# Kernel optimization log

Measured on AMD Instinct MI355X. Metric: run time of the kernel, lower is better.

The kernel has to match this reference:

```python
import jax, jax.numpy as jnp
import numpy as np

NUM_EMBEDDINGS = 2048
EMBEDDING_DIM = 256
COMMITMENT_COST = 0.25


def setup_inputs() -> dict:
    key = jax.random.key(0)
    k1, k2 = jax.random.split(key)
    z_e = jax.random.normal(k1, (64, EMBEDDING_DIM, 32, 32), dtype=jnp.float32)
    # nn.Embedding weight initialized uniform(-1/K, 1/K)
    bound = 1.0 / NUM_EMBEDDINGS
    codebook = jax.random.uniform(k2, (NUM_EMBEDDINGS, EMBEDDING_DIM),
                                  dtype=jnp.float32, minval=-bound, maxval=bound)
    return {"z_e": z_e, "codebook": codebook}


def reference(z_e, codebook):
    B, C, H, W = z_e.shape  # C == embedding_dim
    K = codebook.shape[0]
    sg = jax.lax.stop_gradient

    # [B, C, H, W] -> [B*H*W, C]
    z_e_flat = jnp.transpose(z_e, (0, 2, 3, 1)).reshape(-1, C)

    # squared L2 distances: ||z||^2 - 2 z E^T + ||E||^2  -> [N, K]
    distances = (jnp.sum(z_e_flat ** 2, axis=1, keepdims=True)
                 - 2.0 * jnp.matmul(z_e_flat, codebook.T)
                 + jnp.sum(codebook ** 2, axis=1))
    indices = jnp.argmin(distances, axis=1)  # [N]

    encodings = jax.nn.one_hot(indices, K, dtype=z_e_flat.dtype)  # [N, K]
    z_q_flat = codebook[indices]  # [N, C] embedding gather
    z_q = jnp.transpose(z_q_flat.reshape(B, H, W, C), (0, 3, 1, 2))

    codebook_loss = jnp.mean((z_q_flat - sg(z_e_flat)) ** 2)
    commitment_loss = jnp.mean((sg(z_q_flat) - z_e_flat) ** 2)
    loss = codebook_loss + COMMITMENT_COST * commitment_loss

    e_mean = jnp.mean(encodings, axis=0)  # [K]
    perplexity = jnp.exp(-jnp.sum(e_mean * jnp.log(e_mean + 1e-10)))

    # straight-through estimator
    z_q_st = z_e + sg(z_q - z_e)
    return z_q_st, loss, perplexity, encodings
```

## Files before the change

### kernel.cpp

```cpp
#include <hip/hip_runtime.h>
#include <hip/hip_bf16.h>
#include <math.h>

#define NTOT 65536
#define KCB  2048
#define CDIM 256
#define HW   1024

#define OUT_LOSS 16777216
#define OUT_PERP 16777217
#define OUT_ENC  16777218

#define ZB_OFF_F  16777232
#define CBB_OFF_F 33554448

#define WS_SROW 0
#define WS_CK   262144
#define WS_IDX  270336
#define WS_CNT  532480
#define WS_PART 540672

#define MARGIN 3e-3f
#define CAP 4096

typedef __attribute__((ext_vector_type(8))) short short8;
typedef __attribute__((ext_vector_type(4))) float f32x4;

__device__ inline unsigned enc_f(float x) {
    unsigned u = __float_as_uint(x);
    return (u & 0x80000000u) ? ~u : (u | 0x80000000u);
}
__device__ inline float dec_f(unsigned e) {
    unsigned u = (e & 0x80000000u) ? (e ^ 0x80000000u) : ~e;
    return __uint_as_float(u);
}

__device__ inline void lds_min_u64(unsigned long long* p, unsigned long long v) {
    unsigned long long old = *p;
    while (v < old) {
        unsigned long long assumed = old;
        old = atomicCAS(p, assumed, v);
        if (old == assumed) break;
    }
}

__global__ __launch_bounds__(256) void k_prep(const float* __restrict__ z, const float* __restrict__ cb,
                                              ushort* __restrict__ zb, ushort* __restrict__ cbb,
                                              float* __restrict__ ck, float* __restrict__ srow,
                                              int* __restrict__ cntK) {
    __shared__ float tile[64][65];
    const int tid = threadIdx.x;
    const int bid = blockIdx.x;
    if (bid < 512) {
        int wv = tid >> 6, lane = tid & 63;
        int r = bid * 4 + wv;
        const float* row = cb + (size_t)r * CDIM;
        float4 v = *(const float4*)(row + lane * 4);
        ushort4 o;
        __hip_bfloat16 h;
        h = __float2bfloat16(v.x); o.x = *(ushort*)&h;
        h = __float2bfloat16(v.y); o.y = *(ushort*)&h;
        h = __float2bfloat16(v.z); o.z = *(ushort*)&h;
        h = __float2bfloat16(v.w); o.w = *(ushort*)&h;
        *(ushort4*)(cbb + (size_t)r * CDIM + lane * 4) = o;
        float s = v.x*v.x + v.y*v.y + v.z*v.z + v.w*v.w;
        for (int off = 32; off >= 1; off >>= 1) s += __shfl_down(s, off, 64);
        if (lane == 0) ck[r] = s;
        if (lane == 1) cntK[r] = 0;
    } else if (bid < 768) {
        int n = (bid - 512) * 256 + tid;
        int b = n >> 10, hw = n & 1023;
        const float* base = z + (size_t)b * (CDIM * HW) + hw;
        float s = 0.f;
#pragma unroll 8
        for (int c = 0; c < CDIM; ++c) { float v = base[(size_t)c * HW]; s = fmaf(v, v, s); }
        srow[n] = s;
    } else {
        int zbid = bid - 768;
        int hwT = zbid & 15, cT = (zbid >> 4) & 3, b = zbid >> 6;
        int c0 = cT * 64, hw0 = hwT * 64;
        int w = tid >> 6, hw = tid & 63;
#pragma unroll
        for (int l = 0; l < 16; ++l) {
            int c = l * 4 + w;
            tile[c][hw] = z[((size_t)b * CDIM + (c0 + c)) * HW + hw0 + hw];
        }
        __syncthreads();
        int r = tid >> 2, g = tid & 3;
        union { ushort u[16]; int4 v[2]; } pk;
#pragma unroll
        for (int j = 0; j < 16; ++j) {
            __hip_bfloat16 h = __float2bfloat16(tile[g * 16 + j][r]);
            pk.u[j] = *(ushort*)&h;
        }
        size_t n = (size_t)b * HW + hw0 + r;
        ushort* dst = zb + n * CDIM + c0 + g * 16;
        *(int4*)(dst) = pk.v[0];
        *(int4*)(dst + 8) = pk.v[1];
    }
}

__device__ __forceinline__ void tile_mfma(const ushort* __restrict__ cbb, int kb, int col, int quad,
                                          const short8 (&areg)[4][8], f32x4 (&acc)[4][2]) {
#pragma unroll
    for (int nt = 0; nt < 4; ++nt)
#pragma unroll
        for (int kt = 0; kt < 2; ++kt)
            acc[nt][kt] = (f32x4){0.f, 0.f, 0.f, 0.f};
#pragma unroll
    for (int kt = 0; kt < 2; ++kt) {
        short8 bfrag[8];
#pragma unroll
        for (int cs = 0; cs < 8; ++cs)
            bfrag[cs] = *(const short8*)(cbb + ((size_t)(kb + kt * 16 + col)) * CDIM + cs * 32 + quad * 8);
#pragma unroll
        for (int nt = 0; nt < 4; ++nt)
#pragma unroll
            for (int cs = 0; cs < 8; ++cs)
                acc[nt][kt] = __builtin_amdgcn_mfma_f32_16x16x32_bf16(areg[nt][cs], bfrag[cs], acc[nt][kt], 0, 0, 0);
    }
}

__global__ __launch_bounds__(256, 2) void k_mfma_argmin(
    const ushort* __restrict__ zb, const ushort* __restrict__ cbb,
    const float* __restrict__ z, const float* __restrict__ cb,
    const float* __restrict__ srow, const float* __restrict__ ckg,
    int* __restrict__ indices, int* __restrict__ cntK)
{
    __shared__ unsigned rowminU[64];
    __shared__ int   candRK[CAP];
    __shared__ float candD[CAP];
    __shared__ int   cnt;
    __shared__ float thrF[64];
    __shared__ unsigned long long best[64];

    const int tid = threadIdx.x;
    const int w = tid >> 6, lane = tid & 63;
    const int col = lane & 15, quad = lane >> 4;
    const int n0 = blockIdx.x * 64;

    short8 areg[4][8];
#pragma unroll
    for (int nt = 0; nt < 4; ++nt)
#pragma unroll
        for (int cs = 0; cs < 8; ++cs)
            areg[nt][cs] = *(const short8*)(zb + ((size_t)(n0 + nt * 16 + col)) * CDIM + cs * 32 + quad * 8);

    if (tid < 64) { rowminU[tid] = 0xFFFFFFFFu; best[tid] = ~0ull; }
    if (tid == 0) cnt = 0;
    float gmin[16];
#pragma unroll
    for (int s = 0; s < 16; ++s) gmin[s] = INFINITY;
    __syncthreads();

    {
        f32x4 acc[4][2];
        tile_mfma(cbb, w * 32, col, quad, areg, acc);
#pragma unroll
        for (int kt = 0; kt < 2; ++kt) {
            const float ckv = ckg[w * 32 + kt * 16 + col];
#pragma unroll
            for (int nt = 0; nt < 4; ++nt)
#pragma unroll
                for (int r = 0; r < 4; ++r) {
                    float dt = fmaf(-2.0f, acc[nt][kt][r], ckv);
                    const int s = nt * 4 + r;
                    if (dt < gmin[s]) {
                        gmin[s] = dt;
                        atomicMin(&rowminU[nt * 16 + quad * 4 + r], enc_f(dt));
                    }
                }
        }
    }
    __syncthreads();

    int npass = 1;
    float thr[16];
    for (int pass = 0; pass < npass; ++pass) {
        for (int k0 = 0; k0 < KCB; k0 += 128) {
            const int kb = k0 + w * 32;
            if (pass == 0) {
#pragma unroll
                for (int s = 0; s < 16; ++s) {
                    int row = (s >> 2) * 16 + quad * 4 + (s & 3);
                    gmin[s] = fminf(gmin[s], dec_f(rowminU[row]));
                }
            }
            f32x4 acc[4][2];
            tile_mfma(cbb, kb, col, quad, areg, acc);
#pragma unroll
            for (int kt = 0; kt < 2; ++kt) {
                const int k = kb + kt * 16 + col;
                const float ckv = ckg[k];
#pragma unroll
                for (int nt = 0; nt < 4; ++nt)
#pragma unroll
                    for (int r = 0; r < 4; ++r) {
                        float dt = fmaf(-2.0f, acc[nt][kt][r], ckv);
                        const int s = nt * 4 + r;
                        const int row = nt * 16 + quad * 4 + r;
                        if (pass == 0) {
                            if (dt < gmin[s]) {
                                gmin[s] = dt;
                                atomicMin(&rowminU[row], enc_f(dt));
                            }
                            if (dt <= gmin[s] + MARGIN) {
                                int p = atomicAdd(&cnt, 1);
                                if (p < CAP) { candRK[p] = (row << 16) | k; candD[p] = dt; }
                            }
                        } else if (dt <= thr[s]) {
                            int p = atomicAdd(&cnt, 1);
                            if (p < CAP) { candRK[p] = (row << 16) | k; candD[p] = dt; }
                        }
                    }
            }
        }
        __syncthreads();
        if (pass == 0) {
#pragma unroll
            for (int s = 0; s < 16; ++s)
                thr[s] = dec_f(rowminU[(s >> 2) * 16 + quad * 4 + (s & 3)]) + MARGIN;
            if (cnt > CAP) {
                npass = 2;
                __syncthreads();
                if (tid == 0) cnt = 0;
                __syncthreads();
            }
        }
    }
    if (tid < 64) thrF[tid] = dec_f(rowminU[tid]) + MARGIN;
    __syncthreads();

    const int b = n0 >> 10, hw0 = n0 & 1023;
    const int nc = min(cnt, CAP);
    for (int t = tid; t < nc; t += 256) {
        const int rc = candRK[t];
        const int row = rc >> 16, k = rc & 0xFFFF;
        if (candD[t] > thrF[row]) continue;
        const float* zp = z + (size_t)b * (CDIM * HW) + hw0 + row;
        const float* cp = cb + (size_t)k * CDIM;
        float m = 0.f;
#pragma unroll 8
        for (int c = 0; c < CDIM; ++c) m = fmaf(zp[(size_t)c << 10], cp[c], m);
        float d = (srow[n0 + row] - 2.0f * m) + ckg[k];
        unsigned long long pk = ((unsigned long long)__float_as_uint(d) << 32) | (unsigned)k;
        lds_min_u64(&best[row], pk);
    }
    __syncthreads();
    if (tid < 64) {
        int bk = (int)(best[tid] & 0xFFFFFFFFull);
        indices[n0 + tid] = bk;
        atomicAdd(&cntK[bk], 1);
    }
}

__global__ __launch_bounds__(256, 2) void k_gather(const float* __restrict__ z, const float* __restrict__ cb,
                                                   const int* __restrict__ idx, float* __restrict__ out0,
                                                   double* __restrict__ part) {
    __shared__ float qt[CDIM * 64];
    __shared__ double sh[256];
    const int tid = threadIdx.x;
    const int nl = tid & 63, cg = tid >> 6;
    const int n0 = blockIdx.x * 64;
    const int b = n0 >> 10, hw0 = n0 & 1023;
    const int k = idx[n0 + nl];
    const float* crow = cb + (size_t)k * CDIM + cg * 64;
#pragma unroll
    for (int j4 = 0; j4 < 16; ++j4) {
        float4 v = *(const float4*)(crow + j4 * 4);
        int c = cg * 64 + j4 * 4;
        qt[(c + 0) * 64 + nl] = v.x;
        qt[(c + 1) * 64 + nl] = v.y;
        qt[(c + 2) * 64 + nl] = v.z;
        qt[(c + 3) * 64 + nl] = v.w;
    }
    __syncthreads();
    double acc = 0.0;
    const size_t ebase = ((size_t)b * CDIM) * HW + hw0 + nl;
#pragma unroll 4
    for (int j = 0; j < 64; ++j) {
        int c = cg * 64 + j;
        size_t e = ebase + ((size_t)c << 10);
        float ze = z[e];
        float q = qt[c * 64 + nl];
        float d = q - ze;
        out0[e] = ze + d;
        acc += (double)d * (double)d;
    }
    sh[tid] = acc;
    __syncthreads();
    for (int s = 128; s > 0; s >>= 1) {
        if (tid < s) sh[tid] += sh[tid + s];
        __syncthreads();
    }
    if (tid == 0) part[blockIdx.x] = sh[0];
}

__global__ __launch_bounds__(256) void k_encodings(const int* __restrict__ idx, float4* __restrict__ p4,
                                                   float* __restrict__ tail) {
    __shared__ int sidx[17];
    const int tid = threadIdx.x;
    const size_t g0 = (size_t)blockIdx.x * 8192;
    const long f0 = 4L * (long)g0 - 2;
    int nlo = (int)(f0 >> 11); if (nlo < 0) nlo = 0;
    if (tid < 17) { int n = nlo + tid; sidx[tid] = (n < NTOT) ? idx[n] : -1; }
    __syncthreads();
    const float4 zv = make_float4(0.f, 0.f, 0.f, 0.f);
    for (int i = 0; i < 32; ++i) {
        size_t g = g0 + (size_t)i * 256 + tid;
        long fe = 4L * (long)g - 2;
        float4 v = zv;
        if (fe < 0) {
            int kk = sidx[0];
            if (kk == 0) v.z = 1.f;
            if (kk == 1) v.w = 1.f;
        } else {
            int n = (int)(fe >> 11);
            int k0c = (int)(fe & 2047);
            if (k0c >= 2045) {
#pragma unroll
                for (int j = 0; j < 4; ++j) {
                    long fej = fe + j;
                    int nj = (int)(fej >> 11);
                    int kj = (int)(fej & 2047);
                    int li = nj - nlo;
                    int kk = (li >= 0 && li < 17) ? sidx[li] : -2;
                    ((float*)&v)[j] = (kk == kj) ? 1.f : 0.f;
                }
            } else {
                int d = sidx[n - nlo] - k0c;
                if (d >= 0 && d < 4) ((float*)&v)[d] = 1.f;
            }
        }
        p4[g] = v;
    }
    if (blockIdx.x == 0 && tid == 0) {
        int kk = idx[NTOT - 1];
        tail[0] = (kk == 2046) ? 1.f : 0.f;
        tail[1] = (kk == 2047) ? 1.f : 0.f;
    }
}

__global__ __launch_bounds__(256) void k_finalize(const double* __restrict__ part, const int* __restrict__ cnt,
                                                  float* __restrict__ out) {
    __shared__ double sh[256];
    double a = 0.0;
    for (int i = threadIdx.x; i < 1024; i += 256) a += part[i];
    sh[threadIdx.x] = a; __syncthreads();
    for (int s = 128; s > 0; s >>= 1) { if (threadIdx.x < s) sh[threadIdx.x] += sh[threadIdx.x + s]; __syncthreads(); }
    double total = sh[0];
    __syncthreads();
    double p = 0.0;
    for (int i = threadIdx.x; i < 2048; i += 256) {
        double pm = (double)cnt[i] / 65536.0;
        p += pm * log(pm + 1e-10);
    }
    sh[threadIdx.x] = p; __syncthreads();
    for (int s = 128; s > 0; s >>= 1) { if (threadIdx.x < s) sh[threadIdx.x] += sh[threadIdx.x + s]; __syncthreads(); }
    if (threadIdx.x == 0) {
        double mean = total / ((double)NTOT * (double)CDIM);
        out[OUT_LOSS] = (float)(mean * 1.25);
        out[OUT_PERP] = (float)exp(-sh[0]);
    }
}

extern "C" void kernel_launch(void* const* d_in, const int* in_sizes, int n_in,
                              void* d_out, int out_size, void* d_ws, size_t ws_size,
                              hipStream_t stream) {
    const float* z  = (const float*)d_in[0];
    const float* cb = (const float*)d_in[1];
    float* out = (float*)d_out;
    char* ws = (char*)d_ws;
    float*  srow = (float*)(ws + WS_SROW);
    float*  ck   = (float*)(ws + WS_CK);
    int*    idx  = (int*)(ws + WS_IDX);
    int*    cnt  = (int*)(ws + WS_CNT);
    double* part = (double*)(ws + WS_PART);
    ushort* zb  = (ushort*)(out + ZB_OFF_F);
    ushort* cbb = (ushort*)(out + CBB_OFF_F);

    hipLaunchKernelGGL(k_prep,        dim3(4864), dim3(256), 0, stream, z, cb, zb, cbb, ck, srow, cnt);
    hipLaunchKernelGGL(k_mfma_argmin, dim3(1024), dim3(256), 0, stream, zb, cbb, z, cb, srow, ck, idx, cnt);
    hipLaunchKernelGGL(k_gather,      dim3(1024), dim3(256), 0, stream, z, cb, idx, out, part);
    hipLaunchKernelGGL(k_encodings,   dim3(4096), dim3(256), 0, stream, idx, (float4*)(out + OUT_LOSS),
                       out + (OUT_LOSS + (size_t)33554432 * 4));
    hipLaunchKernelGGL(k_finalize,    dim3(1),    dim3(256), 0, stream, part, cnt, out);
}
```

Before: 1.004 ms.

## Replace two-pass candidate scan with per-lane top-2 tracking and single MFMA pass

The approximate argmin kernel no longer uses a warm-up tile plus shared-memory atomicMin updates and per-element candidate appends inside the MFMA loop. Each lane now keeps the best and second-best distance and index per row in registers. Rows are reduced with shuffles and per-wave shared slots to build a threshold, and candidates are emitted only afterward: the best index alone, or all 32 of the lane's column indices when the second-best lies within the margin. This removes atomics and branches from the hot loop, halves the candidate buffer and drops candD. The cost is a heavier fallback: a full fp32 exact scan over all 2048 codes for the block when candidates overflow.

```diff
diff --git a/kernel.cpp b/kernel.cpp
--- a/kernel.cpp
+++ b/kernel.cpp
@@ -21,7 +21,7 @@
 #define WS_PART 540672
 
 #define MARGIN 3e-3f
-#define CAP 4096
+#define CAP 2048
 
 typedef __attribute__((ext_vector_type(8))) short short8;
 typedef __attribute__((ext_vector_type(4))) float f32x4;
@@ -100,38 +100,17 @@
     }
 }
 
-__device__ __forceinline__ void tile_mfma(const ushort* __restrict__ cbb, int kb, int col, int quad,
-                                          const short8 (&areg)[4][8], f32x4 (&acc)[4][2]) {
-#pragma unroll
-    for (int nt = 0; nt < 4; ++nt)
-#pragma unroll
-        for (int kt = 0; kt < 2; ++kt)
-            acc[nt][kt] = (f32x4){0.f, 0.f, 0.f, 0.f};
-#pragma unroll
-    for (int kt = 0; kt < 2; ++kt) {
-        short8 bfrag[8];
-#pragma unroll
-        for (int cs = 0; cs < 8; ++cs)
-            bfrag[cs] = *(const short8*)(cbb + ((size_t)(kb + kt * 16 + col)) * CDIM + cs * 32 + quad * 8);
-#pragma unroll
-        for (int nt = 0; nt < 4; ++nt)
-#pragma unroll
-            for (int cs = 0; cs < 8; ++cs)
-                acc[nt][kt] = __builtin_amdgcn_mfma_f32_16x16x32_bf16(areg[nt][cs], bfrag[cs], acc[nt][kt], 0, 0, 0);
-    }
-}
-
 __global__ __launch_bounds__(256, 2) void k_mfma_argmin(
     const ushort* __restrict__ zb, const ushort* __restrict__ cbb,
     const float* __restrict__ z, const float* __restrict__ cb,
     const float* __restrict__ srow, const float* __restrict__ ckg,
     int* __restrict__ indices, int* __restrict__ cntK)
 {
-    __shared__ unsigned rowminU[64];
+    __shared__ unsigned long long wmin[4][64];
+    __shared__ float thrRow[64];
     __shared__ int   candRK[CAP];
-    __shared__ float candD[CAP];
     __shared__ int   cnt;
-    __shared__ float thrF[64];
+    __shared__ int   allscan;
     __shared__ unsigned long long best[64];
 
     const int tid = threadIdx.x;
@@ -146,97 +125,95 @@
         for (int cs = 0; cs < 8; ++cs)
             areg[nt][cs] = *(const short8*)(zb + ((size_t)(n0 + nt * 16 + col)) * CDIM + cs * 32 + quad * 8);
 
-    if (tid < 64) { rowminU[tid] = 0xFFFFFFFFu; best[tid] = ~0ull; }
-    if (tid == 0) cnt = 0;
-    float gmin[16];
-#pragma unroll
-    for (int s = 0; s < 16; ++s) gmin[s] = INFINITY;
-    __syncthreads();
-
-    {
-        f32x4 acc[4][2];
-        tile_mfma(cbb, w * 32, col, quad, areg, acc);
+    float m1[16], m2[16]; int k1[16];
+#pragma unroll
+    for (int s = 0; s < 16; ++s) { m1[s] = INFINITY; m2[s] = INFINITY; k1[s] = 0; }
+
+    for (int k0 = 0; k0 < KCB; k0 += 128) {
+        const int kb = k0 + w * 32;
 #pragma unroll
         for (int kt = 0; kt < 2; ++kt) {
-            const float ckv = ckg[w * 32 + kt * 16 + col];
+            const int kk = kb + kt * 16 + col;
+            const ushort* bbase = cbb + (size_t)kk * CDIM + quad * 8;
+            short8 bfrag[8];
+#pragma unroll
+            for (int cs = 0; cs < 8; ++cs) bfrag[cs] = *(const short8*)(bbase + cs * 32);
+            f32x4 acc[4];
+#pragma unroll
+            for (int nt = 0; nt < 4; ++nt) acc[nt] = (f32x4){0.f, 0.f, 0.f, 0.f};
+#pragma unroll
+            for (int cs = 0; cs < 8; ++cs)
+#pragma unroll
+                for (int nt = 0; nt < 4; ++nt)
+                    acc[nt] = __builtin_amdgcn_mfma_f32_16x16x32_bf16(areg[nt][cs], bfrag[cs], acc[nt], 0, 0, 0);
+            const float ckv = ckg[kk];
 #pragma unroll
             for (int nt = 0; nt < 4; ++nt)
 #pragma unroll
                 for (int r = 0; r < 4; ++r) {
-                    float dt = fmaf(-2.0f, acc[nt][kt][r], ckv);
+                    float dt = fmaf(-2.0f, acc[nt][r], ckv);
                     const int s = nt * 4 + r;
-                    if (dt < gmin[s]) {
-                        gmin[s] = dt;
-                        atomicMin(&rowminU[nt * 16 + quad * 4 + r], enc_f(dt));
-                    }
+                    bool c = dt < m1[s];
+                    m2[s] = fminf(m2[s], fmaxf(dt, m1[s]));
+                    m1[s] = fminf(m1[s], dt);
+                    k1[s] = c ? kk : k1[s];
                 }
         }
     }
-    __syncthreads();
-
-    int npass = 1;
-    float thr[16];
-    for (int pass = 0; pass < npass; ++pass) {
-        for (int k0 = 0; k0 < KCB; k0 += 128) {
-            const int kb = k0 + w * 32;
-            if (pass == 0) {
-#pragma unroll
-                for (int s = 0; s < 16; ++s) {
-                    int row = (s >> 2) * 16 + quad * 4 + (s & 3);
-                    gmin[s] = fminf(gmin[s], dec_f(rowminU[row]));
+
+#pragma unroll
+    for (int s = 0; s < 16; ++s) {
+        unsigned long long v = ((unsigned long long)enc_f(m1[s]) << 32) | (unsigned)k1[s];
+#pragma unroll
+        for (int m = 1; m <= 8; m <<= 1) {
+            unsigned long long o = __shfl_xor(v, m, 64);
+            v = (o < v) ? o : v;
+        }
+        if (col == 0) wmin[w][(s >> 2) * 16 + quad * 4 + (s & 3)] = v;
+    }
+    if (tid == 0) { cnt = 0; allscan = 0; }
+    if (tid < 64) best[tid] = ~0ull;
+    __syncthreads();
+    if (tid < 64) {
+        unsigned long long v = wmin[0][tid];
+        unsigned long long o = wmin[1][tid]; v = (o < v) ? o : v;
+        o = wmin[2][tid]; v = (o < v) ? o : v;
+        o = wmin[3][tid]; v = (o < v) ? o : v;
+        thrRow[tid] = dec_f((unsigned)(v >> 32)) + MARGIN;
+    }
+    __syncthreads();
+
+#pragma unroll
+    for (int s = 0; s < 16; ++s) {
+        const int row = (s >> 2) * 16 + quad * 4 + (s & 3);
+        const float thr = thrRow[row];
+        if (m1[s] <= thr) {
+            int p = atomicAdd(&cnt, 1);
+            if (p < CAP) candRK[p] = (row << 16) | k1[s];
+        }
+        if (m2[s] <= thr) {
+            const int kt = s & 1;
+            (void)kt;
+            int p = atomicAdd(&cnt, 32);
+            if (p + 32 <= CAP) {
+#pragma unroll
+                for (int k0i = 0; k0i < 16; ++k0i) {
+                    int kbase = k0i * 128 + w * 32 + col;
+                    candRK[p + 2 * k0i]     = (row << 16) | kbase;
+                    candRK[p + 2 * k0i + 1] = (row << 16) | (kbase + 16);
                 }
             }
-            f32x4 acc[4][2];
-            tile_mfma(cbb, kb, col, quad, areg, acc);
-#pragma unroll
-            for (int kt = 0; kt < 2; ++kt) {
-                const int k = kb + kt * 16 + col;
-                const float ckv = ckg[k];
-#pragma unroll
-                for (int nt = 0; nt < 4; ++nt)
-#pragma unroll
-                    for (int r = 0; r < 4; ++r) {
-                        float dt = fmaf(-2.0f, acc[nt][kt][r], ckv);
-                        const int s = nt * 4 + r;
-                        const int row = nt * 16 + quad * 4 + r;
-                        if (pass == 0) {
-                            if (dt < gmin[s]) {
-                                gmin[s] = dt;
-                                atomicMin(&rowminU[row], enc_f(dt));
-                            }
-                            if (dt <= gmin[s] + MARGIN) {
-                                int p = atomicAdd(&cnt, 1);
-                                if (p < CAP) { candRK[p] = (row << 16) | k; candD[p] = dt; }
-                            }
-                        } else if (dt <= thr[s]) {
-                            int p = atomicAdd(&cnt, 1);
-                            if (p < CAP) { candRK[p] = (row << 16) | k; candD[p] = dt; }
-                        }
-                    }
-            }
-        }
-        __syncthreads();
-        if (pass == 0) {
-#pragma unroll
-            for (int s = 0; s < 16; ++s)
-                thr[s] = dec_f(rowminU[(s >> 2) * 16 + quad * 4 + (s & 3)]) + MARGIN;
-            if (cnt > CAP) {
-                npass = 2;
-                __syncthreads();
-                if (tid == 0) cnt = 0;
-                __syncthreads();
-            }
-        }
-    }
-    if (tid < 64) thrF[tid] = dec_f(rowminU[tid]) + MARGIN;
-    __syncthreads();
+        }
+    }
+    __syncthreads();
+    if (cnt > CAP) { if (tid == 0) allscan = 1; }
+    __syncthreads();
+    const int nc = allscan ? 0 : min(cnt, CAP);
 
     const int b = n0 >> 10, hw0 = n0 & 1023;
-    const int nc = min(cnt, CAP);
     for (int t = tid; t < nc; t += 256) {
         const int rc = candRK[t];
         const int row = rc >> 16, k = rc & 0xFFFF;
-        if (candD[t] > thrF[row]) continue;
         const float* zp = z + (size_t)b * (CDIM * HW) + hw0 + row;
         const float* cp = cb + (size_t)k * CDIM;
         float m = 0.f;
@@ -245,6 +222,22 @@
         float d = (srow[n0 + row] - 2.0f * m) + ckg[k];
         unsigned long long pk = ((unsigned long long)__float_as_uint(d) << 32) | (unsigned)k;
         lds_min_u64(&best[row], pk);
+    }
+    if (allscan) {
+        for (int row = 0; row < 64; ++row) {
+            const float sr = srow[n0 + row];
+            const float* zp = z + (size_t)b * (CDIM * HW) + hw0 + row;
+            for (int kq = 0; kq < 8; ++kq) {
+                int k = kq * 256 + tid;
+                const float* cp = cb + (size_t)k * CDIM;
+                float m = 0.f;
+#pragma unroll 8
+                for (int c = 0; c < CDIM; ++c) m = fmaf(zp[(size_t)c << 10], cp[c], m);
+                float d = (sr - 2.0f * m) + ckg[k];
+                unsigned long long pk = ((unsigned long long)__float_as_uint(d) << 32) | (unsigned)k;
+                lds_min_u64(&best[row], pk);
+            }
+        }
     }
     __syncthreads();
     if (tid < 64) {
```

New measurement: 926.0 us. -7.8%, faster.
